# Kernel tuning notes

Measured on AMD Instinct MI355X. Metric: run time of the kernel, lower is better.

## Reference

```python
import jax, jax.numpy as jnp
import numpy as np


def l2norm(t, eps=1e-12):
    # matches F.normalize(p=2, dim=-1): divide by norm clamped to eps
    n = jnp.linalg.norm(t, axis=-1, keepdims=True)
    return t / jnp.maximum(n, eps)


def setup_inputs() -> dict:
    key = jax.random.key(0)
    kx, ke = jax.random.split(key)
    B, N, D, C = 8, 1024, 256, 8192
    x = jax.random.normal(kx, (B, N, D), dtype=jnp.float32)
    # codebook initialized l2-normalized, as in __init__ (kmeans_init=False)
    embed = l2norm(jax.random.normal(ke, (1, C, D), dtype=jnp.float32))
    return {"x": x, "embed": embed}


def reference(x, embed):
    # x: [B, N, D]; ndim < 4 -> add codebook dim h=1
    xh = x[None]                                   # [1, B, N, D]
    h, b, n, d = xh.shape
    flat = l2norm(xh.reshape(h, b * n, d))         # [1, B*N, D]
    e = l2norm(embed)                              # [1, C, D]
    # cosine-similarity distances
    dist = jnp.einsum('hnd,hcd->hnc', flat, e)     # [1, B*N, C]
    # sample_codebook_temp == 0 -> plain argmax
    idx = jnp.argmax(dist, axis=-1).reshape(h, b, n)  # [1, B, N]
    # batched_embedding: gather UN-normalized codebook rows
    quantize = jax.vmap(lambda em, ix: em[ix])(embed, idx)  # [1, B, N, D]
    # needs_codebook_dim -> strip leading dim
    return quantize[0], idx[0]
```

## Files before the change

### kernel.cpp

```cpp
#include <hip/hip_runtime.h>
#include <math.h>

#define QROWS 8192
#define DDIM  256
#define CCNT  8192
#define BM    256
#define BN    256
#define BK    32
#define CBLKS (CCNT / BN)

typedef __attribute__((ext_vector_type(4))) float f32x4;
typedef __attribute__((ext_vector_type(8))) short bf16x8;

__device__ __forceinline__ unsigned short f2bf(float f) {
    unsigned u = __float_as_uint(f);
    u += 0x7fffu + ((u >> 16) & 1u);
    return (unsigned short)(u >> 16);
}
__device__ __forceinline__ unsigned u32max(unsigned a, unsigned b) { return a > b ? a : b; }
__device__ __forceinline__ unsigned u32min(unsigned a, unsigned b) { return a < b ? a : b; }

__device__ __forceinline__ unsigned key32(float v, unsigned enc) {
    unsigned u = __float_as_uint(v);
    unsigned s = (unsigned)((int)u >> 31);
    return ((u ^ (s | 0x80000000u)) & 0xFFFFFF00u) | enc;
}

__global__ void k_prep(const float* __restrict__ x, unsigned short* __restrict__ xb,
                       const float* __restrict__ e, unsigned short* __restrict__ eb) {
    const int bid = blockIdx.x;
    if (bid < 1024) {
        const int i = (bid * 256 + threadIdx.x) * 8;
        const float4 f0 = *reinterpret_cast<const float4*>(x + i);
        const float4 f1 = *reinterpret_cast<const float4*>(x + i + 4);
        uint4 o;
        o.x = f2bf(f0.x) | ((unsigned)f2bf(f0.y) << 16);
        o.y = f2bf(f0.z) | ((unsigned)f2bf(f0.w) << 16);
        o.z = f2bf(f1.x) | ((unsigned)f2bf(f1.y) << 16);
        o.w = f2bf(f1.z) | ((unsigned)f2bf(f1.w) << 16);
        *reinterpret_cast<uint4*>(xb + i) = o;
    } else {
        const int row  = (bid - 1024) * 4 + (threadIdx.x >> 6);
        const int lane = threadIdx.x & 63;
        const float4 v = *reinterpret_cast<const float4*>(e + (size_t)row * DDIM + lane * 4);
        float s = v.x * v.x + v.y * v.y + v.z * v.z + v.w * v.w;
        #pragma unroll
        for (int off = 1; off < 64; off <<= 1) s += __shfl_xor(s, off);
        const float inv = 1.0f / fmaxf(sqrtf(s), 1e-12f);
        ushort4 o;
        o.x = f2bf(v.x * inv); o.y = f2bf(v.y * inv);
        o.z = f2bf(v.z * inv); o.w = f2bf(v.w * inv);
        *reinterpret_cast<ushort4*>(eb + (size_t)row * DDIM + lane * 4) = o;
    }
}

#define GLOAD_LDS(g, s) \
    __builtin_amdgcn_global_load_lds((const __attribute__((address_space(1))) void*)(g), \
                                     (__attribute__((address_space(3))) void*)(s), 16, 0, 0)

#define SBAR do { asm volatile("" ::: "memory"); __builtin_amdgcn_s_barrier(); \
                  asm volatile("" ::: "memory"); } while (0)
#define WAIT_LGKM0 do { asm volatile("s_waitcnt lgkmcnt(0)" ::: "memory"); \
                        __builtin_amdgcn_sched_barrier(0); } while (0)
#define WAIT_VM4 do { asm volatile("s_waitcnt vmcnt(4)" ::: "memory"); \
                      __builtin_amdgcn_sched_barrier(0); } while (0)
#define WAIT_VM0 do { asm volatile("s_waitcnt vmcnt(0)" ::: "memory"); \
                      __builtin_amdgcn_sched_barrier(0); } while (0)

__launch_bounds__(512, 2)
__global__ void k_gemm(const unsigned short* __restrict__ xb,
                       const unsigned short* __restrict__ eb,
                       unsigned* pout ) {
    __shared__ __align__(16) char smem[65536];

    const int tid = threadIdx.x;
    const int w = tid >> 6, l = tid & 63;
    const int wr = w >> 2, wc = w & 3;
    const int lg = l >> 4, lr = l & 15;
    const int bx = blockIdx.x, by = blockIdx.y;
    const int n0 = by * BM, c0 = bx * BN;

    const f32x4 zero = {0.f, 0.f, 0.f, 0.f};
    f32x4 acc[8][4];
    #pragma unroll
    for (int i = 0; i < 8; ++i)
        #pragma unroll
        for (int j = 0; j < 4; ++j) acc[i][j] = zero;

    const int srow = tid >> 2;
    const int schk = (tid & 3) ^ ((tid >> 3) & 3);
    const char* gA = (const char*)xb + (size_t)(n0 + srow) * 512 + schk * 16;
    const char* gB = (const char*)eb + (size_t)(c0 + srow) * 512 + schk * 16;
    const int wb = w * 1024;

#define STAGE(slot, t) do {                                                  \
    GLOAD_LDS(gA + (t) * 64,         smem + (slot) * 32768 + wb);            \
    GLOAD_LDS(gA + (t) * 64 + 65536, smem + (slot) * 32768 + 8192 + wb);     \
    GLOAD_LDS(gB + (t) * 64,         smem + (slot) * 32768 + 16384 + wb);    \
    GLOAD_LDS(gB + (t) * 64 + 65536, smem + (slot) * 32768 + 24576 + wb);    \
} while (0)

    const int chkx = (lr >> 1) & 3;
    const int aoff = (wr * 128 + lr) * 64 + ((lg ^ chkx) * 16);
    const int boff = 16384 + (wc * 64 + lr) * 64 + ((lg ^ chkx) * 16);

    bf16x8 a[8], b[4];
#define READS(slot) do {                                                                  \
    const char* base_ = smem + (slot) * 32768;                                            \
    _Pragma("unroll") for (int mi = 0; mi < 8; ++mi)                                      \
        a[mi] = *reinterpret_cast<const bf16x8*>(base_ + aoff + mi * 1024);               \
    _Pragma("unroll") for (int nj = 0; nj < 4; ++nj)                                      \
        b[nj] = *reinterpret_cast<const bf16x8*>(base_ + boff + nj * 1024);               \
} while (0)

#define MMAS() do {                                                          \
    __builtin_amdgcn_s_setprio(1);                                           \
    _Pragma("unroll") for (int mi = 0; mi < 8; ++mi)                         \
      _Pragma("unroll") for (int nj = 0; nj < 4; ++nj)                       \
        acc[mi][nj] = __builtin_amdgcn_mfma_f32_16x16x32_bf16(a[mi], b[nj], acc[mi][nj], 0, 0, 0); \
    __builtin_amdgcn_s_setprio(0);                                           \
} while (0)

    STAGE(0, 0);
    STAGE(1, 1);
    WAIT_VM4; SBAR;

    #pragma unroll
    for (int t = 0; t < 8; ++t) {
        const int slot = t & 1;
        READS(slot);
        WAIT_LGKM0;
        SBAR;
        if (t + 2 < 8) STAGE(slot, t + 2);
        MMAS();
        if (t < 7) {
            if (t < 6) { WAIT_VM4; } else { WAIT_VM0; }
            SBAR;
        }
    }
    __syncthreads();

    uint2* T = (uint2*)smem;
    const int slotW = wc * 16 + lr;
    const unsigned encb = 255u - (unsigned)(wc * 64 + lr);
    #pragma unroll
    for (int half = 0; half < 2; ++half) {
        #pragma unroll
        for (int m = 0; m < 4; ++m) {
            const int mi = half * 4 + m;
            #pragma unroll
            for (int r = 0; r < 4; ++r) {
                unsigned q0 = key32(acc[mi][0][r], encb);
                unsigned q1 = key32(acc[mi][1][r], encb - 16);
                unsigned q2 = key32(acc[mi][2][r], encb - 32);
                unsigned q3 = key32(acc[mi][3][r], encb - 48);
                const unsigned m01 = u32max(q0, q1), n01 = u32min(q0, q1);
                const unsigned m23 = u32max(q2, q3), n23 = u32min(q2, q3);
                const unsigned t1 = u32max(m01, m23);
                const unsigned t2 = u32max(u32min(m01, m23), u32max(n01, n23));
                const int cr = wr * 64 + m * 16 + lg * 4 + r;
                uint2 p; p.x = t1; p.y = t2;
                T[cr * 64 + (slotW ^ (cr & 15))] = p;
            }
        }
        __syncthreads();
        {
            const int cr = tid >> 2, q = tid & 3;
            unsigned T1 = 0, T2 = 0;
            #pragma unroll
            for (int i = 0; i < 16; ++i) {
                const uint2 p = T[cr * 64 + ((q * 16 + i) ^ (cr & 15))];
                const unsigned n1 = u32max(T1, p.x);
                const unsigned lo = u32min(T1, p.x);
                T2 = u32max(T2, u32max(lo, p.y));
                T1 = n1;
            }
            #pragma unroll
            for (int off = 1; off < 4; off <<= 1) {
                const unsigned o1 = __shfl_xor(T1, off);
                const unsigned o2 = __shfl_xor(T2, off);
                const unsigned n1 = u32max(T1, o1);
                const unsigned lo = u32min(T1, o1);
                T2 = u32max(u32max(T2, o2), lo);
                T1 = n1;
            }
            if (q == 0) {
                const int row = n0 + (cr >> 6) * 128 + half * 64 + (cr & 63);
                uint2 o; o.x = T1; o.y = T2;
                *reinterpret_cast<uint2*>(pout + (size_t)row * 256 + bx * 2) = o;
            }
        }
        if (half == 0) __syncthreads();
    }
#undef STAGE
#undef READS
#undef MMAS
}

__global__ void k_fixup(const unsigned* pk,
                        const float* __restrict__ x, const float* __restrict__ e,
                        float* out) {
    const int row = blockIdx.x * 4 + (threadIdx.x >> 6);
    const int t   = threadIdx.x & 63;
    const unsigned k = pk[(size_t)row * 256 + t];
    const int col0 = (t >> 1) * 256 + 255 - (int)(k & 255u);
    unsigned long long kk = ((unsigned long long)(k & 0xFFFFFF00u) << 32) | (unsigned)(~col0);

    int cand[4];
    #pragma unroll
    for (int p = 0; p < 4; ++p) {
        unsigned long long m = kk;
        #pragma unroll
        for (int off = 1; off < 64; off <<= 1) {
            const unsigned long long o = __shfl_xor(m, off);
            if (o > m) m = o;
        }
        cand[p] = (int)(~(unsigned)m) & (CCNT - 1);
        if (kk == m) kk = 0ull;
    }

    const float4 xv = *reinterpret_cast<const float4*>(x + (size_t)row * DDIM + t * 4);
    float best = -INFINITY; int bc = 0x7fffffff;
    #pragma unroll
    for (int p = 0; p < 4; ++p) {
        const int c = cand[p];
        const float4 ev = *reinterpret_cast<const float4*>(e + (size_t)c * DDIM + t * 4);
        float d  = xv.x * ev.x + xv.y * ev.y + xv.z * ev.z + xv.w * ev.w;
        float ss = ev.x * ev.x + ev.y * ev.y + ev.z * ev.z + ev.w * ev.w;
        #pragma unroll
        for (int off = 1; off < 64; off <<= 1) {
            d  += __shfl_xor(d, off);
            ss += __shfl_xor(ss, off);
        }
        const float v = d * (1.0f / fmaxf(sqrtf(ss), 1e-12f));
        if (v > best || (v == best && c < bc)) { best = v; bc = c; }
    }

    if (t == 0) out[(size_t)QROWS * DDIM + row] = (float)bc;
    const float4 q = *reinterpret_cast<const float4*>(e + (size_t)bc * DDIM + t * 4);
    *reinterpret_cast<float4*>(out + (size_t)row * DDIM + t * 4) = q;
}

extern "C" void kernel_launch(void* const* d_in, const int* in_sizes, int n_in,
                              void* d_out, int out_size, void* d_ws, size_t ws_size,
                              hipStream_t stream) {
    const float* x = (const float*)d_in[0];
    const float* e = (const float*)d_in[1];
    float* out = (float*)d_out;
    char* ws = (char*)d_ws;

    unsigned short* xb = (unsigned short*)ws;
    unsigned short* eb = (unsigned short*)(ws + (size_t)4 * 1024 * 1024);

    k_prep<<<3072, 256, 0, stream>>>(x, xb, e, eb);
    dim3 g2(CBLKS, QROWS / BM);
    k_gemm<<<g2, 512, 0, stream>>>(xb, eb, (unsigned*)d_out);
    k_fixup<<<QROWS / 4, 256, 0, stream>>>((const unsigned*)d_out, x, e, out);
}
```

Measured before the change: 68.32 us.

## Double GEMM K-tile to 64 with 128KB dynamic LDS and split MFMA phases

Raises the GEMM K-tile from 32 to 64 and moves to 128KB of dynamic shared memory, so the K=256 loop runs in 4 steps instead of 8 with wider 128-byte swizzled rows. Each step is split into four read/MFMA phases, with separate A-half and B reads between barriers. The aim is fewer loop iterations and less barrier and wait overhead per unit of MFMA work. The trade-off is that 128KB of LDS per block likely limits the CU to one resident block instead of two. The new schedule also adds many barriers and waits for all loads each step, which may expose memory latency.

```diff
diff --git a/kernel.cpp b/kernel.cpp
--- a/kernel.cpp
+++ b/kernel.cpp
@@ -6,7 +6,7 @@
 #define CCNT  8192
 #define BM    256
 #define BN    256
-#define BK    32
+#define BK    64
 #define CBLKS (CCNT / BN)
 
 typedef __attribute__((ext_vector_type(4))) float f32x4;
@@ -62,16 +62,14 @@
                   asm volatile("" ::: "memory"); } while (0)
 #define WAIT_LGKM0 do { asm volatile("s_waitcnt lgkmcnt(0)" ::: "memory"); \
                         __builtin_amdgcn_sched_barrier(0); } while (0)
-#define WAIT_VM4 do { asm volatile("s_waitcnt vmcnt(4)" ::: "memory"); \
-                      __builtin_amdgcn_sched_barrier(0); } while (0)
-#define WAIT_VM0 do { asm volatile("s_waitcnt vmcnt(0)" ::: "memory"); \
-                      __builtin_amdgcn_sched_barrier(0); } while (0)
+#define WAIT_VM(n) do { asm volatile("s_waitcnt vmcnt(" #n ")" ::: "memory"); \
+                        __builtin_amdgcn_sched_barrier(0); } while (0)
 
 __launch_bounds__(512, 2)
 __global__ void k_gemm(const unsigned short* __restrict__ xb,
                        const unsigned short* __restrict__ eb,
                        unsigned* pout ) {
-    __shared__ __align__(16) char smem[65536];
+    extern __shared__ __align__(16) char smem[];
 
     const int tid = threadIdx.x;
     const int w = tid >> 6, l = tid & 63;
@@ -87,56 +85,61 @@
         #pragma unroll
         for (int j = 0; j < 4; ++j) acc[i][j] = zero;
 
-    const int srow = tid >> 2;
-    const int schk = (tid & 3) ^ ((tid >> 3) & 3);
-    const char* gA = (const char*)xb + (size_t)(n0 + srow) * 512 + schk * 16;
-    const char* gB = (const char*)eb + (size_t)(c0 + srow) * 512 + schk * 16;
-    const int wb = w * 1024;
-
-#define STAGE(slot, t) do {                                                  \
-    GLOAD_LDS(gA + (t) * 64,         smem + (slot) * 32768 + wb);            \
-    GLOAD_LDS(gA + (t) * 64 + 65536, smem + (slot) * 32768 + 8192 + wb);     \
-    GLOAD_LDS(gB + (t) * 64,         smem + (slot) * 32768 + 16384 + wb);    \
-    GLOAD_LDS(gB + (t) * 64 + 65536, smem + (slot) * 32768 + 24576 + wb);    \
-} while (0)
-
-    const int chkx = (lr >> 1) & 3;
-    const int aoff = (wr * 128 + lr) * 64 + ((lg ^ chkx) * 16);
-    const int boff = 16384 + (wc * 64 + lr) * 64 + ((lg ^ chkx) * 16);
-
-    bf16x8 a[8], b[4];
-#define READS(slot) do {                                                                  \
-    const char* base_ = smem + (slot) * 32768;                                            \
-    _Pragma("unroll") for (int mi = 0; mi < 8; ++mi)                                      \
-        a[mi] = *reinterpret_cast<const bf16x8*>(base_ + aoff + mi * 1024);               \
-    _Pragma("unroll") for (int nj = 0; nj < 4; ++nj)                                      \
-        b[nj] = *reinterpret_cast<const bf16x8*>(base_ + boff + nj * 1024);               \
-} while (0)
-
-#define MMAS() do {                                                          \
-    __builtin_amdgcn_s_setprio(1);                                           \
-    _Pragma("unroll") for (int mi = 0; mi < 8; ++mi)                         \
-      _Pragma("unroll") for (int nj = 0; nj < 4; ++nj)                       \
-        acc[mi][nj] = __builtin_amdgcn_mfma_f32_16x16x32_bf16(a[mi], b[nj], acc[mi][nj], 0, 0, 0); \
-    __builtin_amdgcn_s_setprio(0);                                           \
+    const int aBase = (wr * 128 + lr) * 128;
+    const int bBase = 32768 + (wc * 64 + lr) * 128;
+    const int pc0 = (lg ^ (lr & 7)) * 16;
+    const int pc1 = pc0 ^ 64;
+
+    const int srow = l >> 3;
+    const int scl  = (l & 7) ^ srow;
+    const char* gA = (const char*)xb + (size_t)(n0 + w * 8 + srow) * 512 + scl * 16;
+    const char* gB = (const char*)eb + (size_t)(c0 + w * 8 + srow) * 512 + scl * 16;
+    const int ldsw = w * 1024;
+
+#define STAGE(bufoff, kt) do {                                                         \
+    _Pragma("unroll") for (int q_ = 0; q_ < 4; ++q_)                                   \
+        GLOAD_LDS(gA + q_ * 32768 + (kt) * 128, smem + (bufoff) + q_ * 8192 + ldsw);   \
+    _Pragma("unroll") for (int q_ = 0; q_ < 4; ++q_)                                   \
+        GLOAD_LDS(gB + q_ * 32768 + (kt) * 128, smem + (bufoff) + 32768 + q_ * 8192 + ldsw); \
+} while (0)
+
+    bf16x8 a[4], b[4];
+#define READ_A(bufoff, h, pc) do {                                                     \
+    _Pragma("unroll") for (int mi_ = 0; mi_ < 4; ++mi_)                                \
+        a[mi_] = *reinterpret_cast<const bf16x8*>(smem + (bufoff) + aBase + ((h) * 4 + mi_) * 2048 + (pc)); \
+} while (0)
+#define READ_B(bufoff, pc) do {                                                        \
+    _Pragma("unroll") for (int nj_ = 0; nj_ < 4; ++nj_)                                \
+        b[nj_] = *reinterpret_cast<const bf16x8*>(smem + (bufoff) + bBase + nj_ * 2048 + (pc)); \
+} while (0)
+#define MMA(h) do {                                                                    \
+    __builtin_amdgcn_s_setprio(1);                                                     \
+    _Pragma("unroll") for (int mi_ = 0; mi_ < 4; ++mi_)                                \
+      _Pragma("unroll") for (int nj_ = 0; nj_ < 4; ++nj_)                              \
+        acc[(h) * 4 + mi_][nj_] = __builtin_amdgcn_mfma_f32_16x16x32_bf16(a[mi_], b[nj_], acc[(h) * 4 + mi_][nj_], 0, 0, 0); \
+    __builtin_amdgcn_s_setprio(0);                                                     \
 } while (0)
 
     STAGE(0, 0);
-    STAGE(1, 1);
-    WAIT_VM4; SBAR;
-
-    #pragma unroll
-    for (int t = 0; t < 8; ++t) {
-        const int slot = t & 1;
-        READS(slot);
-        WAIT_LGKM0;
+    STAGE(65536, 1);
+    WAIT_VM(8);
+    SBAR;
+
+    #pragma unroll
+    for (int kt = 0; kt < 4; ++kt) {
+        const int bo = (kt & 1) * 65536;
+        READ_B(bo, pc0); READ_A(bo, 0, pc0);
+        if (kt == 1) STAGE(0, 2);
+        if (kt == 2) STAGE(65536, 3);
+        SBAR; WAIT_LGKM0; MMA(0); SBAR;
+        READ_A(bo, 1, pc0);
+        SBAR; WAIT_LGKM0; MMA(1); SBAR;
+        READ_B(bo, pc1); READ_A(bo, 0, pc1);
+        SBAR; WAIT_LGKM0; MMA(0); SBAR;
+        READ_A(bo, 1, pc1);
+        SBAR; WAIT_LGKM0; MMA(1);
+        if (kt < 3) WAIT_VM(0);
         SBAR;
-        if (t + 2 < 8) STAGE(slot, t + 2);
-        MMAS();
-        if (t < 7) {
-            if (t < 6) { WAIT_VM4; } else { WAIT_VM0; }
-            SBAR;
-        }
     }
     __syncthreads();
 
@@ -193,8 +196,9 @@
         if (half == 0) __syncthreads();
     }
 #undef STAGE
-#undef READS
-#undef MMAS
+#undef READ_A
+#undef READ_B
+#undef MMA
 }
 
 __global__ void k_fixup(const unsigned* pk,
@@ -252,8 +256,11 @@
     unsigned short* xb = (unsigned short*)ws;
     unsigned short* eb = (unsigned short*)(ws + (size_t)4 * 1024 * 1024);
 
+    hipFuncSetAttribute(reinterpret_cast<const void*>(k_gemm),
+                        hipFuncAttributeMaxDynamicSharedMemorySize, 131072);
+
     k_prep<<<3072, 256, 0, stream>>>(x, xb, e, eb);
     dim3 g2(CBLKS, QROWS / BM);
-    k_gemm<<<g2, 512, 0, stream>>>(xb, eb, (unsigned*)d_out);
+    k_gemm<<<g2, 512, 131072, stream>>>(xb, eb, (unsigned*)d_out);
     k_fixup<<<QROWS / 4, 256, 0, stream>>>((const unsigned*)d_out, x, e, out);
 }
```

Measured after the change: 67.99 us. No clear change (-0.5%).
